# Kernel tuning notes

Measured on AMD Instinct MI355X. Metric: run time of the kernel, lower is better.

Reference implementation:

```python
import jax, jax.numpy as jnp
import numpy as np

TAYLOR_ORDER = 16      # Taylor terms after scaling (||A_s|| <= 0.5 -> machine precision)
MAX_SQUARINGS = 16     # fixed upper bound on squaring steps (jit-friendly)


def batched_expm(A):
    """Vectorized scaling-and-squaring matrix exponential for A of shape [..., n, n].

    Replaces the original per-item torch.linalg.matrix_exp Python loop with one
    fused batched computation (same math: exp(Q*t)).
    """
    n = A.shape[-1]
    I = jnp.eye(n, dtype=A.dtype)
    # per-matrix infinity norm [...,]
    nrm = jnp.max(jnp.sum(jnp.abs(A), axis=-1), axis=-1)
    # number of squarings so that scaled norm <= 0.5
    s = jnp.clip(jnp.ceil(jnp.log2(jnp.maximum(nrm, 1e-30) / 0.5)), 0.0, float(MAX_SQUARINGS))
    As = A * jnp.exp2(-s)[..., None, None]
    # Taylor series: P = I + As + As^2/2! + ...
    P = jnp.broadcast_to(I, A.shape)
    term = P
    for k in range(1, TAYLOR_ORDER + 1):
        term = jnp.matmul(term, As) / k
        P = P + term
    # undo scaling: square s times (data-dependent count via masked squaring)
    s_b = s[..., None, None]
    for i in range(MAX_SQUARINGS):
        P = jnp.where(s_b > i, jnp.matmul(P, P), P)
    return P


def setup_inputs() -> dict:
    key = jax.random.key(0)
    k1, k2 = jax.random.split(key)
    rate_matrix = jax.random.normal(k1, (64, 32768, 4, 4), dtype=jnp.float32)
    time = jax.random.uniform(k2, (64,), dtype=jnp.float32)
    return {"rate_matrix": rate_matrix, "time": time}


def reference(rate_matrix, time):
    # Qt = rate_matrix[i, j] * time[i], batched over (batch, seq_len)
    Qt = rate_matrix * time[:, None, None, None]
    return batched_expm(Qt)  # [B, S, 4, 4] transition probability matrices
```

## Files before the change

### kernel.cpp

```cpp
#include <hip/hip_runtime.h>
#include <math.h>


typedef float f4 __attribute__((ext_vector_type(4)));

__device__ __forceinline__ void mm4(float* __restrict__ D,
                                    const float* __restrict__ X,
                                    const float* __restrict__ Y)
{
    #pragma unroll
    for (int i = 0; i < 4; ++i) {
        const float x0 = X[4*i+0], x1 = X[4*i+1];
        const float x2 = X[4*i+2], x3 = X[4*i+3];
        #pragma unroll
        for (int j = 0; j < 4; ++j) {
            float v = x0 * Y[j];
            v = __builtin_fmaf(x1, Y[4+j],  v);
            v = __builtin_fmaf(x2, Y[8+j],  v);
            v = __builtin_fmaf(x3, Y[12+j], v);
            D[4*i+j] = v;
        }
    }
}

__global__ void __launch_bounds__(256) expm4_kernel(
    const float* __restrict__ A,
    const float* __restrict__ tvec,
    float* __restrict__ out,
    int M, int S)
{
    const int m = blockIdx.x * 256 + threadIdx.x;
    if (m >= M) return;

    const float t = tvec[m / S];

    float a[16];
    const f4* Ap = reinterpret_cast<const f4*>(A) + (size_t)m * 4;
    #pragma unroll
    for (int i = 0; i < 4; ++i) {
        f4 v = Ap[i];
        a[4*i+0] = v.x * t;
        a[4*i+1] = v.y * t;
        a[4*i+2] = v.z * t;
        a[4*i+3] = v.w * t;
    }

    float nrm = 0.0f;
    #pragma unroll
    for (int i = 0; i < 4; ++i) {
        float rs = fabsf(a[4*i+0]) + fabsf(a[4*i+1])
                 + fabsf(a[4*i+2]) + fabsf(a[4*i+3]);
        nrm = fmaxf(nrm, rs);
    }

    float sf = ceilf(log2f(fmaxf(nrm, 1e-30f) * 2.0f));
    sf = fminf(fmaxf(sf, 0.0f), 16.0f);
    const int   si    = (int)sf;
    const float scale = exp2f(-sf);
    #pragma unroll
    for (int i = 0; i < 16; ++i) a[i] *= scale;

    float A2[16], A3[16];
    mm4(A2, a, a);
    mm4(A3, A2, a);

    constexpr float C2 = 1.0f/2.0f,    C3 = 1.0f/6.0f;
    constexpr float C4 = 1.0f/24.0f,   C5 = 1.0f/120.0f;
    constexpr float C6 = 1.0f/720.0f,  C7 = 1.0f/5040.0f;
    constexpr float C8 = 1.0f/40320.0f, C9 = 1.0f/362880.0f;

    float G[16], HI[16], PI[16];
    #pragma unroll
    for (int i = 0; i < 16; ++i) {
        G[i]  = __builtin_fmaf(C9, A3[i],
                __builtin_fmaf(C8, A2[i], C7 * a[i]));
        HI[i] = __builtin_fmaf(C5, A2[i], C4 * a[i]);
        PI[i] = __builtin_fmaf(C2, A2[i], a[i]);
    }
    G[0]  += C6; G[5]  += C6; G[10] += C6; G[15] += C6;
    HI[0] += C3; HI[5] += C3; HI[10] += C3; HI[15] += C3;
    PI[0] += 1.0f; PI[5] += 1.0f; PI[10] += 1.0f; PI[15] += 1.0f;

    float H[16];
    #pragma unroll
    for (int i = 0; i < 4; ++i) {
        const float g0 = G[4*i+0], g1 = G[4*i+1];
        const float g2 = G[4*i+2], g3 = G[4*i+3];
        #pragma unroll
        for (int j = 0; j < 4; ++j) {
            float v = HI[4*i+j];
            v = __builtin_fmaf(g0, A3[j],    v);
            v = __builtin_fmaf(g1, A3[4+j],  v);
            v = __builtin_fmaf(g2, A3[8+j],  v);
            v = __builtin_fmaf(g3, A3[12+j], v);
            H[4*i+j] = v;
        }
    }

    float P[16];
    #pragma unroll
    for (int i = 0; i < 4; ++i) {
        const float h0 = H[4*i+0], h1 = H[4*i+1];
        const float h2 = H[4*i+2], h3 = H[4*i+3];
        #pragma unroll
        for (int j = 0; j < 4; ++j) {
            float v = PI[4*i+j];
            v = __builtin_fmaf(h0, A3[j],    v);
            v = __builtin_fmaf(h1, A3[4+j],  v);
            v = __builtin_fmaf(h2, A3[8+j],  v);
            v = __builtin_fmaf(h3, A3[12+j], v);
            P[4*i+j] = v;
        }
    }

    int it = si;
    while (it >= 2) {
        float Q[16];
        mm4(Q, P, P);
        mm4(P, Q, Q);
        it -= 2;
    }
    if (it) {
        float Q[16];
        mm4(Q, P, P);
        #pragma unroll
        for (int i = 0; i < 16; ++i) P[i] = Q[i];
    }

    f4* Op = reinterpret_cast<f4*>(out) + (size_t)m * 4;
    #pragma unroll
    for (int i = 0; i < 4; ++i) {
        f4 v;
        v.x = P[4*i+0]; v.y = P[4*i+1]; v.z = P[4*i+2]; v.w = P[4*i+3];
        __builtin_nontemporal_store(v, Op + i);
    }
}

extern "C" void kernel_launch(void* const* d_in, const int* in_sizes, int n_in,
                              void* d_out, int out_size, void* d_ws, size_t ws_size,
                              hipStream_t stream) {
    const float* A    = (const float*)d_in[0];
    const float* tvec = (const float*)d_in[1];
    float* out        = (float*)d_out;

    const int B = in_sizes[1];
    const int M = in_sizes[0] / 16;
    const int S = M / B;

    const int threads = 256;
    const int blocks  = (M + threads - 1) / threads;
    expm4_kernel<<<blocks, threads, 0, stream>>>(A, tvec, out, M, S);
}
```

Baseline: 280.5 us.

## Process two matrices per thread with early loads and block-uniform time lookup

Each thread now handles two 4x4 matrices, issuing both matrices' global loads before computing so more memory requests are in flight per thread. When the sequence length divides evenly into blocks, the time scalar is read once per block instead of through a per-thread integer division. The time factor is folded into the scaling constant, and the norm is computed on the raw matrix times |t|. Stores change from nontemporal to regular, and the two-matrix path raises register pressure and halves the grid size.

After: 237.3 us. 1.18x faster.

```diff
diff --git a/kernel.cpp b/kernel.cpp
--- a/kernel.cpp
+++ b/kernel.cpp
@@ -3,6 +3,10 @@
 
 
 typedef float f4 __attribute__((ext_vector_type(4)));
+
+constexpr int NMAT = 2;
+constexpr int TPB  = 256;
+constexpr int MPB  = NMAT * TPB;
 
 __device__ __forceinline__ void mm4(float* __restrict__ D,
                                     const float* __restrict__ X,
@@ -23,50 +27,38 @@
     }
 }
 
-__global__ void __launch_bounds__(256) expm4_kernel(
-    const float* __restrict__ A,
-    const float* __restrict__ tvec,
-    float* __restrict__ out,
-    int M, int S)
+__device__ __forceinline__ void expm4_one(const f4 r[4], float t, f4 o[4])
 {
-    const int m = blockIdx.x * 256 + threadIdx.x;
-    if (m >= M) return;
-
-    const float t = tvec[m / S];
-
-    float a[16];
-    const f4* Ap = reinterpret_cast<const f4*>(A) + (size_t)m * 4;
-    #pragma unroll
-    for (int i = 0; i < 4; ++i) {
-        f4 v = Ap[i];
-        a[4*i+0] = v.x * t;
-        a[4*i+1] = v.y * t;
-        a[4*i+2] = v.z * t;
-        a[4*i+3] = v.w * t;
-    }
-
+    const float at = fabsf(t);
     float nrm = 0.0f;
     #pragma unroll
     for (int i = 0; i < 4; ++i) {
-        float rs = fabsf(a[4*i+0]) + fabsf(a[4*i+1])
-                 + fabsf(a[4*i+2]) + fabsf(a[4*i+3]);
+        float rs = fabsf(r[i].x) + fabsf(r[i].y) + fabsf(r[i].z) + fabsf(r[i].w);
         nrm = fmaxf(nrm, rs);
     }
+    nrm *= at;
 
     float sf = ceilf(log2f(fmaxf(nrm, 1e-30f) * 2.0f));
     sf = fminf(fmaxf(sf, 0.0f), 16.0f);
-    const int   si    = (int)sf;
-    const float scale = exp2f(-sf);
+    const int   si = (int)sf;
+    const float c  = t * exp2f(-sf);
+
+    float a[16];
     #pragma unroll
-    for (int i = 0; i < 16; ++i) a[i] *= scale;
+    for (int i = 0; i < 4; ++i) {
+        a[4*i+0] = r[i].x * c;
+        a[4*i+1] = r[i].y * c;
+        a[4*i+2] = r[i].z * c;
+        a[4*i+3] = r[i].w * c;
+    }
 
     float A2[16], A3[16];
     mm4(A2, a, a);
     mm4(A3, A2, a);
 
-    constexpr float C2 = 1.0f/2.0f,    C3 = 1.0f/6.0f;
-    constexpr float C4 = 1.0f/24.0f,   C5 = 1.0f/120.0f;
-    constexpr float C6 = 1.0f/720.0f,  C7 = 1.0f/5040.0f;
+    constexpr float C2 = 1.0f/2.0f,     C3 = 1.0f/6.0f;
+    constexpr float C4 = 1.0f/24.0f,    C5 = 1.0f/120.0f;
+    constexpr float C6 = 1.0f/720.0f,   C7 = 1.0f/5040.0f;
     constexpr float C8 = 1.0f/40320.0f, C9 = 1.0f/362880.0f;
 
     float G[16], HI[16], PI[16];
@@ -127,12 +119,58 @@
         for (int i = 0; i < 16; ++i) P[i] = Q[i];
     }
 
-    f4* Op = reinterpret_cast<f4*>(out) + (size_t)m * 4;
     #pragma unroll
     for (int i = 0; i < 4; ++i) {
-        f4 v;
-        v.x = P[4*i+0]; v.y = P[4*i+1]; v.z = P[4*i+2]; v.w = P[4*i+3];
-        __builtin_nontemporal_store(v, Op + i);
+        f4 v; v.x = P[4*i+0]; v.y = P[4*i+1]; v.z = P[4*i+2]; v.w = P[4*i+3];
+        o[i] = v;
+    }
+}
+
+__global__ void __launch_bounds__(TPB) expm4_kernel(
+    const float* __restrict__ A,
+    const float* __restrict__ tvec,
+    float* __restrict__ out,
+    int M, int S, int s_blocks)
+{
+    const int tid = threadIdx.x;
+    const long long mat0 = (long long)blockIdx.x * MPB;
+    const long long m0 = mat0 + tid;
+    const long long m1 = m0 + TPB;
+
+    float t0, t1;
+    if (s_blocks > 0) {
+        const float t = tvec[blockIdx.x / s_blocks];
+        t0 = t; t1 = t;
+    } else {
+        t0 = tvec[(int)(m0 / S)];
+        t1 = (m1 < M) ? tvec[(int)(m1 / S)] : 0.0f;
+    }
+
+    const f4* Ap = reinterpret_cast<const f4*>(A);
+    f4 r0[4], r1[4];
+    const bool v0 = (m0 < M), v1 = (m1 < M);
+    if (v0) {
+        #pragma unroll
+        for (int k = 0; k < 4; ++k) r0[k] = Ap[m0 * 4 + k];
+    }
+    if (v1) {
+        #pragma unroll
+        for (int k = 0; k < 4; ++k) r1[k] = Ap[m1 * 4 + k];
+    }
+
+    f4* Op = reinterpret_cast<f4*>(out);
+
+    if (v0) {
+        f4 o[4];
+        expm4_one(r0, t0, o);
+        #pragma unroll
+        for (int k = 0; k < 4; ++k) Op[m0 * 4 + k] = o[k];
+    }
+    if (v1) {
+        f4 o[4];
+        expm4_one(r1, t1, o);
+        #pragma unroll
+        for (int k = 0; k < 4; ++k) Op[m1 * 4 + k] = o[k];
     }
 }
 
@@ -147,7 +185,8 @@
     const int M = in_sizes[0] / 16;
     const int S = M / B;
 
-    const int threads = 256;
-    const int blocks  = (M + threads - 1) / threads;
-    expm4_kernel<<<blocks, threads, 0, stream>>>(A, tvec, out, M, S);
+    const int s_blocks = (S % MPB == 0) ? (S / MPB) : 0;
+
+    const int blocks = (M + MPB - 1) / MPB;
+    expm4_kernel<<<blocks, TPB, 0, stream>>>(A, tvec, out, M, S, s_blocks);
 }
```
